# Kernel tuning notes

Measured on AMD Instinct MI355X. Metric: run time of the kernel, lower is better.

Reference implementation:

```python
import jax, jax.numpy as jnp
import numpy as np

N_NODES = 100_000
N_EDGES = 1_000_000
LATENT = 64
HID_ATOM = 256
HID_BOND = 256
RBF_DIM = 32
RBF_DMAX = 10.0
N_ATOM_TYPES = 10
N_CHARGES = 6
N_BOND_ORDERS = 5


def setup_inputs() -> dict:
    key = jax.random.key(0)
    ks = jax.random.split(key, 12)
    positions = jax.random.normal(ks[0], (N_NODES, 3), dtype=jnp.float32) * 5.0
    quantized = jax.random.normal(ks[1], (N_NODES, LATENT), dtype=jnp.float32)
    pair_indices = jax.random.randint(ks[2], (N_EDGES, 2), 0, N_NODES, dtype=jnp.int64)
    s = 0.05
    return {
        "positions": positions,
        "quantized": quantized,
        "pair_indices": pair_indices,
        "aW1": jax.random.normal(ks[3], (LATENT, HID_ATOM), jnp.float32) * s,
        "ab1": jnp.zeros((HID_ATOM,), jnp.float32),
        "aW2": jax.random.normal(ks[4], (HID_ATOM, N_ATOM_TYPES + N_CHARGES), jnp.float32) * s,
        "ab2": jnp.zeros((N_ATOM_TYPES + N_CHARGES,), jnp.float32),
        "bW1": jax.random.normal(ks[5], (LATENT + RBF_DIM, HID_BOND), jnp.float32) * s,
        "bb1": jnp.zeros((HID_BOND,), jnp.float32),
        "bW2": jax.random.normal(ks[6], (HID_BOND, N_BOND_ORDERS), jnp.float32) * s,
        "bb2": jnp.zeros((N_BOND_ORDERS,), jnp.float32),
    }


def _norm_no_nan(x, eps=1e-8):
    # L2 norm over last axis, clamped to avoid NaN gradients at 0
    return jnp.sqrt(jnp.maximum(jnp.sum(x * x, axis=-1), eps))


def _rbf(D, D_min=0.0, D_max=RBF_DMAX, D_count=RBF_DIM):
    mu = jnp.linspace(D_min, D_max, D_count, dtype=D.dtype)  # [D_count]
    sigma = (D_max - D_min) / D_count
    z = (D[..., None] - mu) / sigma
    return jnp.exp(-z * z)  # [E, D_count]


def reference(positions, quantized, pair_indices, aW1, ab1, aW2, ab2, bW1, bb1, bW2, bb2):
    src = pair_indices[:, 0]
    dst = pair_indices[:, 1]
    # pairwise distances -> RBF expansion
    x_i = positions[src]            # [E, 3]
    x_j = positions[dst]
    dists = _rbf(_norm_no_nan(x_i - x_j))  # [E, rbf_dim]
    # atom decoder (per node)
    h = jax.nn.relu(quantized @ aW1 + ab1)
    scalar_logits = h @ aW2 + ab2
    atom_type_logits = scalar_logits[:, :N_ATOM_TYPES]
    atom_charge_logits = scalar_logits[:, N_ATOM_TYPES:]
    # bond decoder (per edge): gathered latent sum concat RBF
    pair_feats = quantized[src] + quantized[dst]           # [E, latent]
    combined = jnp.concatenate([pair_feats, dists], axis=1)  # [E, latent+rbf]
    hb = jax.nn.relu(combined @ bW1 + bb1)
    bond_order_logits = hb @ bW2 + bb2
    return (atom_type_logits, atom_charge_logits, bond_order_logits)
```

## Files before the change

kernel.cpp:

```cpp
#include <hip/hip_runtime.h>
#include <hip/hip_bf16.h>

typedef __bf16 bf16x8 __attribute__((ext_vector_type(8)));
typedef __bf16 bf16x4 __attribute__((ext_vector_type(4)));
typedef float  f32x4  __attribute__((ext_vector_type(4)));

#define N_NODES 100000
#define N_EDGES 1000000
#define LATENT  64
#define HID     256
#define RBF_DIM 32
#define NTYPES  10
#define NCHG    6
#define NBOND   5

#define ATOM_TILES (N_NODES / 32)
#define ANBLK 512

#define ETILE  64
#define ETILES (N_EDGES / ETILE)
#define ENBLK  512

struct __align__(16) ASmem {
    __bf16 qs[32][72];
    __bf16 hsE[32][264];
    float  red[4][2][4][64];
};

template<bool EMIT_QB>
__global__ __launch_bounds__(256, 2) void atom_kernel(
    const float* __restrict__ q,   const float* __restrict__ aW1,
    const float* __restrict__ ab1, const float* __restrict__ aW2,
    const float* __restrict__ ab2, float* __restrict__ outA,
    float* __restrict__ outB,      __bf16* __restrict__ qb)
{
    __shared__ ASmem sm;
    const int t    = threadIdx.x;
    const int w    = t >> 6;
    const int lane = t & 63;
    const int l15  = lane & 15;
    const int hi   = lane >> 4;
    const int wcol = w * 64;

    bf16x8 aw1f[2][4];
    #pragma unroll
    for (int kb = 0; kb < 2; ++kb)
        #pragma unroll
        for (int nt = 0; nt < 4; ++nt) {
            const int nn = wcol + nt * 16 + l15;
            const int k0 = kb * 32 + hi * 8;
            bf16x8 v;
            #pragma unroll
            for (int j = 0; j < 8; ++j) v[j] = (__bf16)aW1[(k0 + j) * HID + nn];
            aw1f[kb][nt] = v;
        }
    bf16x8 aw2f[2];
    #pragma unroll
    for (int kk = 0; kk < 2; ++kk) {
        const int k0 = (w * 2 + kk) * 32 + hi * 8;
        bf16x8 v;
        #pragma unroll
        for (int j = 0; j < 8; ++j) v[j] = (__bf16)aW2[(k0 + j) * 16 + l15];
        aw2f[kk] = v;
    }
    float4 b1v[4];
    #pragma unroll
    for (int nt = 0; nt < 4; ++nt)
        b1v[nt] = *(const float4*)(&ab1[wcol + nt * 16 + hi * 4]);

    const int m_st = t >> 3;
    const int p_st = t & 7;

    for (int tile = blockIdx.x; tile < ATOM_TILES; tile += ANBLK) {
        const int node0 = tile * 32;
        {
            const float* qr = q + (size_t)(node0 + m_st) * 64 + p_st * 8;
            const float4 a0 = *(const float4*)(qr);
            const float4 a1 = *(const float4*)(qr + 4);
            bf16x8 v;
            v[0] = (__bf16)a0.x; v[1] = (__bf16)a0.y; v[2] = (__bf16)a0.z; v[3] = (__bf16)a0.w;
            v[4] = (__bf16)a1.x; v[5] = (__bf16)a1.y; v[6] = (__bf16)a1.z; v[7] = (__bf16)a1.w;
            *(bf16x8*)(&sm.qs[m_st][p_st * 8]) = v;
            if constexpr (EMIT_QB)
                *(bf16x8*)(qb + (size_t)(node0 + m_st) * 64 + p_st * 8) = v;
        }
        __syncthreads();

        f32x4 acc[2][4];
        #pragma unroll
        for (int mt = 0; mt < 2; ++mt)
            #pragma unroll
            for (int nt = 0; nt < 4; ++nt)
                #pragma unroll
                for (int r = 0; r < 4; ++r)
                    acc[mt][nt][r] = ((const float*)&b1v[nt])[r];

        __builtin_amdgcn_s_setprio(1);
        #pragma unroll
        for (int kb = 0; kb < 2; ++kb)
            #pragma unroll
            for (int mt = 0; mt < 2; ++mt) {
                const bf16x8 bq = *(const bf16x8*)((const char*)&sm.qs[0][0]
                                   + (mt * 16 + l15) * 144 + kb * 64 + hi * 16);
                #pragma unroll
                for (int nt = 0; nt < 4; ++nt)
                    acc[mt][nt] = __builtin_amdgcn_mfma_f32_16x16x32_bf16(
                        aw1f[kb][nt], bq, acc[mt][nt], 0, 0, 0);
            }
        __builtin_amdgcn_s_setprio(0);

        #pragma unroll
        for (int mt = 0; mt < 2; ++mt)
            #pragma unroll
            for (int nt = 0; nt < 4; ++nt) {
                bf16x4 hv;
                #pragma unroll
                for (int r = 0; r < 4; ++r)
                    hv[r] = (__bf16)fmaxf(acc[mt][nt][r], 0.f);
                *(bf16x4*)(&sm.hsE[mt * 16 + l15][wcol + nt * 16 + hi * 4]) = hv;
            }
        __syncthreads();

        f32x4 acc2[2];
        {
            f32x4 z = {0.f, 0.f, 0.f, 0.f};
            acc2[0] = z; acc2[1] = z;
        }
        __builtin_amdgcn_s_setprio(1);
        #pragma unroll
        for (int mt = 0; mt < 2; ++mt)
            #pragma unroll
            for (int kk = 0; kk < 2; ++kk) {
                const int kb = w * 2 + kk;
                const bf16x8 af = *(const bf16x8*)((const char*)&sm.hsE[0][0]
                                   + (mt * 16 + l15) * 528 + kb * 64 + hi * 16);
                acc2[mt] = __builtin_amdgcn_mfma_f32_16x16x32_bf16(
                    af, aw2f[kk], acc2[mt], 0, 0, 0);
            }
        __builtin_amdgcn_s_setprio(0);
        #pragma unroll
        for (int mt = 0; mt < 2; ++mt)
            #pragma unroll
            for (int r = 0; r < 4; ++r)
                sm.red[w][mt][r][lane] = acc2[mt][r];
        __syncthreads();

        {
            const int o  = t & 15;
            const int m0 = t >> 4;
            #pragma unroll
            for (int half = 0; half < 2; ++half) {
                const int m  = m0 + half * 16;
                const int mt = m >> 4, rr = m & 15;
                const int hh = rr >> 2, r = rr & 3;
                float s = ab2[o];
                #pragma unroll
                for (int ww = 0; ww < 4; ++ww) s += sm.red[ww][mt][r][hh * 16 + o];
                const int node = node0 + m;
                if (o < NTYPES) outA[node * NTYPES + o] = s;
                else            outB[node * NCHG + (o - NTYPES)] = s;
            }
        }
        __syncthreads();
    }
}

struct __align__(16) ESmem {
    __bf16 comb[ETILE][104];
    __bf16 hsE[ETILE][264];
    __bf16 w2t[16][264];
};

__device__ __forceinline__ void bar_lgkm() {
    asm volatile("s_waitcnt lgkmcnt(0)" ::: "memory");
    __builtin_amdgcn_s_barrier();
}

template<bool USEBF>
__global__ __launch_bounds__(512, 4) void edge_kernel(
    const float* __restrict__ pos, const float* __restrict__ qf,
    const __bf16* __restrict__ qb, const int* __restrict__ pair,
    const float* __restrict__ bW1, const float* __restrict__ bb1,
    const float* __restrict__ bW2, const float* __restrict__ bb2,
    float* __restrict__ outC)
{
    __shared__ ESmem sm;
    const int t    = threadIdx.x;
    const int w    = t >> 6;
    const int lane = t & 63;
    const int l15  = lane & 15;
    const int hi   = lane >> 4;
    const int wcol = w * 32;

    {
        const int o  = t >> 5;
        const int k0 = (t & 31) * 8;
        bf16x8 v;
        #pragma unroll
        for (int j = 0; j < 8; ++j)
            v[j] = (o < NBOND) ? (__bf16)bW2[(k0 + j) * NBOND + o] : (__bf16)0.f;
        *(bf16x8*)(&sm.w2t[o][k0]) = v;
    }

    bf16x8 bw1f[3][2];
    #pragma unroll
    for (int kb = 0; kb < 3; ++kb)
        #pragma unroll
        for (int nt = 0; nt < 2; ++nt) {
            const int nn = wcol + nt * 16 + l15;
            const int k0 = kb * 32 + hi * 8;
            bf16x8 v;
            #pragma unroll
            for (int j = 0; j < 8; ++j) v[j] = (__bf16)bW1[(k0 + j) * HID + nn];
            bw1f[kb][nt] = v;
        }
    float4 b1v[2];
    b1v[0] = *(const float4*)(&bb1[wcol + hi * 4]);
    b1v[1] = *(const float4*)(&bb1[wcol + 16 + hi * 4]);
    const float bb2v = (l15 < NBOND) ? bb2[l15] : 0.f;

    const int e_loc = t >> 3;
    const int p     = t & 7;

    int tile = blockIdx.x;
    int2 pA = ((const int2*)pair)[(size_t)tile * ETILE + e_loc];
    bf16x8 gs, gd;
    float4 fs0, fs1, fd0, fd1;
    float  ps0, ps1, ps2, pd0, pd1, pd2;
    if constexpr (USEBF) {
        gs = *(const bf16x8*)(qb + ((unsigned)pA.x * 64u + (unsigned)(p * 8)));
        gd = *(const bf16x8*)(qb + ((unsigned)pA.y * 64u + (unsigned)(p * 8)));
    } else {
        fs0 = *(const float4*)(qf + ((unsigned)pA.x * 64u + (unsigned)(p * 8)));
        fs1 = *(const float4*)(qf + ((unsigned)pA.x * 64u + (unsigned)(p * 8) + 4u));
        fd0 = *(const float4*)(qf + ((unsigned)pA.y * 64u + (unsigned)(p * 8)));
        fd1 = *(const float4*)(qf + ((unsigned)pA.y * 64u + (unsigned)(p * 8) + 4u));
    }
    ps0 = pos[(unsigned)pA.x * 3u];  ps1 = pos[(unsigned)pA.x * 3u + 1u];  ps2 = pos[(unsigned)pA.x * 3u + 2u];
    pd0 = pos[(unsigned)pA.y * 3u];  pd1 = pos[(unsigned)pA.y * 3u + 1u];  pd2 = pos[(unsigned)pA.y * 3u + 2u];
    {
        const int tn = tile + ENBLK;
        pA = ((const int2*)pair)[(tn < ETILES ? (size_t)tn * ETILE : 0) + e_loc];
    }
    __syncthreads();

    for (; tile < ETILES; tile += ENBLK) {
        const int e0 = tile * ETILE;

        {
            bf16x8 cv;
            if constexpr (USEBF) {
                #pragma unroll
                for (int j = 0; j < 8; ++j)
                    cv[j] = (__bf16)((float)gs[j] + (float)gd[j]);
            } else {
                cv[0] = (__bf16)(fs0.x + fd0.x); cv[1] = (__bf16)(fs0.y + fd0.y);
                cv[2] = (__bf16)(fs0.z + fd0.z); cv[3] = (__bf16)(fs0.w + fd0.w);
                cv[4] = (__bf16)(fs1.x + fd1.x); cv[5] = (__bf16)(fs1.y + fd1.y);
                cv[6] = (__bf16)(fs1.z + fd1.z); cv[7] = (__bf16)(fs1.w + fd1.w);
            }
            *(bf16x8*)(&sm.comb[e_loc][p * 8]) = cv;

            const float dx = ps0 - pd0, dy = ps1 - pd1, dz = ps2 - pd2;
            const float D  = sqrtf(fmaxf(dx * dx + dy * dy + dz * dz, 1e-8f));
            bf16x4 rv;
            #pragma unroll
            for (int j = 0; j < 4; ++j) {
                const float mu = (float)(p * 4 + j) * (10.0f / 31.0f);
                const float z  = (D - mu) * 3.2f;
                rv[j] = (__bf16)__expf(-z * z);
            }
            *(bf16x4*)(&sm.comb[e_loc][64 + p * 4]) = rv;
        }

        {
            const int2 pN = pA;
            if constexpr (USEBF) {
                gs = *(const bf16x8*)(qb + ((unsigned)pN.x * 64u + (unsigned)(p * 8)));
                gd = *(const bf16x8*)(qb + ((unsigned)pN.y * 64u + (unsigned)(p * 8)));
            } else {
                fs0 = *(const float4*)(qf + ((unsigned)pN.x * 64u + (unsigned)(p * 8)));
                fs1 = *(const float4*)(qf + ((unsigned)pN.x * 64u + (unsigned)(p * 8) + 4u));
                fd0 = *(const float4*)(qf + ((unsigned)pN.y * 64u + (unsigned)(p * 8)));
                fd1 = *(const float4*)(qf + ((unsigned)pN.y * 64u + (unsigned)(p * 8) + 4u));
            }
            ps0 = pos[(unsigned)pN.x * 3u];  ps1 = pos[(unsigned)pN.x * 3u + 1u];  ps2 = pos[(unsigned)pN.x * 3u + 2u];
            pd0 = pos[(unsigned)pN.y * 3u];  pd1 = pos[(unsigned)pN.y * 3u + 1u];  pd2 = pos[(unsigned)pN.y * 3u + 2u];
            const int tnn = tile + 2 * ENBLK;
            pA = ((const int2*)pair)[(tnn < ETILES ? (size_t)tnn * ETILE : 0) + e_loc];
        }
        bar_lgkm();

        f32x4 acc[4][2];
        #pragma unroll
        for (int mt = 0; mt < 4; ++mt)
            #pragma unroll
            for (int nt = 0; nt < 2; ++nt)
                #pragma unroll
                for (int r = 0; r < 4; ++r)
                    acc[mt][nt][r] = ((const float*)&b1v[nt])[r];

        __builtin_amdgcn_s_setprio(1);
        #pragma unroll
        for (int kb = 0; kb < 3; ++kb)
            #pragma unroll
            for (int mt = 0; mt < 4; ++mt) {
                const bf16x8 bf = *(const bf16x8*)((const char*)&sm.comb[0][0]
                                   + (mt * 16 + l15) * 208 + kb * 64 + hi * 16);
                acc[mt][0] = __builtin_amdgcn_mfma_f32_16x16x32_bf16(
                    bw1f[kb][0], bf, acc[mt][0], 0, 0, 0);
                acc[mt][1] = __builtin_amdgcn_mfma_f32_16x16x32_bf16(
                    bw1f[kb][1], bf, acc[mt][1], 0, 0, 0);
            }
        __builtin_amdgcn_s_setprio(0);

        #pragma unroll
        for (int mt = 0; mt < 4; ++mt)
            #pragma unroll
            for (int nt = 0; nt < 2; ++nt) {
                bf16x4 hv;
                #pragma unroll
                for (int r = 0; r < 4; ++r)
                    hv[r] = (__bf16)fmaxf(acc[mt][nt][r], 0.f);
                *(bf16x4*)((char*)&sm.hsE[0][0]
                           + (mt * 16 + l15) * 528 + (wcol + nt * 16 + hi * 4) * 2) = hv;
            }
        bar_lgkm();

        if (w < 4) {
            f32x4 a2a, a2b;
            #pragma unroll
            for (int r = 0; r < 4; ++r) { a2a[r] = bb2v; a2b[r] = 0.f; }
            __builtin_amdgcn_s_setprio(1);
            #pragma unroll
            for (int kk = 0; kk < 8; kk += 2) {
                const bf16x8 af0 = *(const bf16x8*)((const char*)&sm.hsE[0][0]
                                    + (w * 16 + l15) * 528 + kk * 64 + hi * 16);
                const bf16x8 bf0 = *(const bf16x8*)((const char*)&sm.w2t[0][0]
                                    + l15 * 528 + kk * 64 + hi * 16);
                a2a = __builtin_amdgcn_mfma_f32_16x16x32_bf16(af0, bf0, a2a, 0, 0, 0);
                const bf16x8 af1 = *(const bf16x8*)((const char*)&sm.hsE[0][0]
                                    + (w * 16 + l15) * 528 + (kk + 1) * 64 + hi * 16);
                const bf16x8 bf1 = *(const bf16x8*)((const char*)&sm.w2t[0][0]
                                    + l15 * 528 + (kk + 1) * 64 + hi * 16);
                a2b = __builtin_amdgcn_mfma_f32_16x16x32_bf16(af1, bf1, a2b, 0, 0, 0);
            }
            __builtin_amdgcn_s_setprio(0);
            if (l15 < NBOND) {
                #pragma unroll
                for (int r = 0; r < 4; ++r)
                    outC[(size_t)(e0 + w * 16 + hi * 4 + r) * NBOND + l15]
                        = a2a[r] + a2b[r];
            }
        }
    }
}

extern "C" void kernel_launch(void* const* d_in, const int* in_sizes, int n_in,
                              void* d_out, int out_size, void* d_ws, size_t ws_size,
                              hipStream_t stream)
{
    const float* pos = (const float*)d_in[0];
    const float* q   = (const float*)d_in[1];
    const int*   pair= (const int*)  d_in[2];
    const float* aW1 = (const float*)d_in[3];
    const float* ab1 = (const float*)d_in[4];
    const float* aW2 = (const float*)d_in[5];
    const float* ab2 = (const float*)d_in[6];
    const float* bW1 = (const float*)d_in[7];
    const float* bb1 = (const float*)d_in[8];
    const float* bW2 = (const float*)d_in[9];
    const float* bb2 = (const float*)d_in[10];

    float* out  = (float*)d_out;
    float* outA = out;
    float* outB = out + (size_t)N_NODES * NTYPES;
    float* outC = out + (size_t)N_NODES * (NTYPES + NCHG);

    const size_t qb_bytes = (size_t)N_NODES * LATENT * sizeof(__bf16);
    const bool use_bf = (ws_size >= qb_bytes);
    __bf16* qb = (__bf16*)d_ws;

    if (use_bf)
        hipLaunchKernelGGL(atom_kernel<true>, dim3(ANBLK), dim3(256), 0, stream,
                           q, aW1, ab1, aW2, ab2, outA, outB, qb);
    else
        hipLaunchKernelGGL(atom_kernel<false>, dim3(ANBLK), dim3(256), 0, stream,
                           q, aW1, ab1, aW2, ab2, outA, outB, qb);

    if (use_bf)
        hipLaunchKernelGGL(edge_kernel<true>, dim3(ENBLK), dim3(512), 0, stream,
                           pos, q, qb, pair, bW1, bb1, bW2, bb2, outC);
    else
        hipLaunchKernelGGL(edge_kernel<false>, dim3(ENBLK), dim3(512), 0, stream,
                           pos, q, qb, pair, bW1, bb1, bW2, bb2, outC);
}
```

Before: 98.99 us.

## Restructure edge kernel into double-buffered 32-edge tiles with per-wave output reduction

```diff
diff --git a/kernel.cpp b/kernel.cpp
--- a/kernel.cpp
+++ b/kernel.cpp
@@ -17,9 +17,9 @@
 #define ATOM_TILES (N_NODES / 32)
 #define ANBLK 512
 
-#define ETILE  64
+#define ETILE  32
 #define ETILES (N_EDGES / ETILE)
-#define ENBLK  512
+#define ENBLK  768
 
 struct __align__(16) ASmem {
     __bf16 qs[32][72];
@@ -95,7 +95,6 @@
                 for (int r = 0; r < 4; ++r)
                     acc[mt][nt][r] = ((const float*)&b1v[nt])[r];
 
-        __builtin_amdgcn_s_setprio(1);
         #pragma unroll
         for (int kb = 0; kb < 2; ++kb)
             #pragma unroll
@@ -107,7 +106,6 @@
                     acc[mt][nt] = __builtin_amdgcn_mfma_f32_16x16x32_bf16(
                         aw1f[kb][nt], bq, acc[mt][nt], 0, 0, 0);
             }
-        __builtin_amdgcn_s_setprio(0);
 
         #pragma unroll
         for (int mt = 0; mt < 2; ++mt)
@@ -126,7 +124,6 @@
             f32x4 z = {0.f, 0.f, 0.f, 0.f};
             acc2[0] = z; acc2[1] = z;
         }
-        __builtin_amdgcn_s_setprio(1);
         #pragma unroll
         for (int mt = 0; mt < 2; ++mt)
             #pragma unroll
@@ -137,7 +134,6 @@
                 acc2[mt] = __builtin_amdgcn_mfma_f32_16x16x32_bf16(
                     af, aw2f[kk], acc2[mt], 0, 0, 0);
             }
-        __builtin_amdgcn_s_setprio(0);
         #pragma unroll
         for (int mt = 0; mt < 2; ++mt)
             #pragma unroll
@@ -166,9 +162,9 @@
 }
 
 struct __align__(16) ESmem {
-    __bf16 comb[ETILE][104];
+    __bf16 comb[2][ETILE][104];
     __bf16 hsE[ETILE][264];
-    __bf16 w2t[16][264];
+    float  red[2][4][2][4][64];
 };
 
 __device__ __forceinline__ void bar_lgkm() {
@@ -177,7 +173,7 @@
 }
 
 template<bool USEBF>
-__global__ __launch_bounds__(512, 4) void edge_kernel(
+__global__ __launch_bounds__(256, 3) void edge_kernel(
     const float* __restrict__ pos, const float* __restrict__ qf,
     const __bf16* __restrict__ qb, const int* __restrict__ pair,
     const float* __restrict__ bW1, const float* __restrict__ bb1,
@@ -190,170 +186,194 @@
     const int lane = t & 63;
     const int l15  = lane & 15;
     const int hi   = lane >> 4;
-    const int wcol = w * 32;
-
-    {
-        const int o  = t >> 5;
-        const int k0 = (t & 31) * 8;
-        bf16x8 v;
-        #pragma unroll
-        for (int j = 0; j < 8; ++j)
-            v[j] = (o < NBOND) ? (__bf16)bW2[(k0 + j) * NBOND + o] : (__bf16)0.f;
-        *(bf16x8*)(&sm.w2t[o][k0]) = v;
-    }
-
-    bf16x8 bw1f[3][2];
+    const int hid0 = w * 64;
+
+    bf16x8 bw1f[3][4];
     #pragma unroll
     for (int kb = 0; kb < 3; ++kb)
         #pragma unroll
-        for (int nt = 0; nt < 2; ++nt) {
-            const int nn = wcol + nt * 16 + l15;
+        for (int nt = 0; nt < 4; ++nt) {
+            const int nn = hid0 + nt * 16 + l15;
             const int k0 = kb * 32 + hi * 8;
             bf16x8 v;
             #pragma unroll
             for (int j = 0; j < 8; ++j) v[j] = (__bf16)bW1[(k0 + j) * HID + nn];
             bw1f[kb][nt] = v;
         }
-    float4 b1v[2];
-    b1v[0] = *(const float4*)(&bb1[wcol + hi * 4]);
-    b1v[1] = *(const float4*)(&bb1[wcol + 16 + hi * 4]);
-    const float bb2v = (l15 < NBOND) ? bb2[l15] : 0.f;
+    bf16x8 w2f[2];
+    #pragma unroll
+    for (int kk = 0; kk < 2; ++kk) {
+        const int k0 = hid0 + kk * 32 + hi * 8;
+        bf16x8 v;
+        #pragma unroll
+        for (int j = 0; j < 8; ++j)
+            v[j] = (l15 < NBOND) ? (__bf16)bW2[(k0 + j) * NBOND + l15] : (__bf16)0.f;
+        w2f[kk] = v;
+    }
+    float4 b1v[4];
+    #pragma unroll
+    for (int nt = 0; nt < 4; ++nt)
+        b1v[nt] = *(const float4*)(&bb1[hid0 + nt * 16 + hi * 4]);
 
     const int e_loc = t >> 3;
     const int p     = t & 7;
 
     int tile = blockIdx.x;
-    int2 pA = ((const int2*)pair)[(size_t)tile * ETILE + e_loc];
     bf16x8 gs, gd;
     float4 fs0, fs1, fd0, fd1;
     float  ps0, ps1, ps2, pd0, pd1, pd2;
-    if constexpr (USEBF) {
-        gs = *(const bf16x8*)(qb + ((unsigned)pA.x * 64u + (unsigned)(p * 8)));
-        gd = *(const bf16x8*)(qb + ((unsigned)pA.y * 64u + (unsigned)(p * 8)));
-    } else {
-        fs0 = *(const float4*)(qf + ((unsigned)pA.x * 64u + (unsigned)(p * 8)));
-        fs1 = *(const float4*)(qf + ((unsigned)pA.x * 64u + (unsigned)(p * 8) + 4u));
-        fd0 = *(const float4*)(qf + ((unsigned)pA.y * 64u + (unsigned)(p * 8)));
-        fd1 = *(const float4*)(qf + ((unsigned)pA.y * 64u + (unsigned)(p * 8) + 4u));
-    }
-    ps0 = pos[(unsigned)pA.x * 3u];  ps1 = pos[(unsigned)pA.x * 3u + 1u];  ps2 = pos[(unsigned)pA.x * 3u + 2u];
-    pd0 = pos[(unsigned)pA.y * 3u];  pd1 = pos[(unsigned)pA.y * 3u + 1u];  pd2 = pos[(unsigned)pA.y * 3u + 2u];
+    int2 pA = ((const int2*)pair)[(size_t)tile * ETILE + e_loc];
+    #define GATHER(pN)                                                            \
+        if constexpr (USEBF) {                                                    \
+            gs = *(const bf16x8*)(qb + ((unsigned)(pN).x * 64u + (unsigned)(p*8)));\
+            gd = *(const bf16x8*)(qb + ((unsigned)(pN).y * 64u + (unsigned)(p*8)));\
+        } else {                                                                  \
+            fs0 = *(const float4*)(qf + ((unsigned)(pN).x * 64u + (unsigned)(p*8)));     \
+            fs1 = *(const float4*)(qf + ((unsigned)(pN).x * 64u + (unsigned)(p*8) + 4u));\
+            fd0 = *(const float4*)(qf + ((unsigned)(pN).y * 64u + (unsigned)(p*8)));     \
+            fd1 = *(const float4*)(qf + ((unsigned)(pN).y * 64u + (unsigned)(p*8) + 4u));\
+        }                                                                         \
+        ps0 = pos[(unsigned)(pN).x * 3u];  ps1 = pos[(unsigned)(pN).x * 3u + 1u]; \
+        ps2 = pos[(unsigned)(pN).x * 3u + 2u];                                    \
+        pd0 = pos[(unsigned)(pN).y * 3u];  pd1 = pos[(unsigned)(pN).y * 3u + 1u]; \
+        pd2 = pos[(unsigned)(pN).y * 3u + 2u];
+
+    #define STAGE(buf)                                                            \
+        {                                                                         \
+            bf16x8 cv;                                                            \
+            if constexpr (USEBF) {                                                \
+                _Pragma("unroll")                                                 \
+                for (int j = 0; j < 8; ++j)                                       \
+                    cv[j] = (__bf16)((float)gs[j] + (float)gd[j]);                \
+            } else {                                                              \
+                cv[0] = (__bf16)(fs0.x + fd0.x); cv[1] = (__bf16)(fs0.y + fd0.y); \
+                cv[2] = (__bf16)(fs0.z + fd0.z); cv[3] = (__bf16)(fs0.w + fd0.w); \
+                cv[4] = (__bf16)(fs1.x + fd1.x); cv[5] = (__bf16)(fs1.y + fd1.y); \
+                cv[6] = (__bf16)(fs1.z + fd1.z); cv[7] = (__bf16)(fs1.w + fd1.w); \
+            }                                                                     \
+            *(bf16x8*)(&sm.comb[buf][e_loc][p * 8]) = cv;                         \
+            const float dx = ps0 - pd0, dy = ps1 - pd1, dz = ps2 - pd2;           \
+            const float D  = sqrtf(fmaxf(dx * dx + dy * dy + dz * dz, 1e-8f));    \
+            bf16x4 rv;                                                            \
+            _Pragma("unroll")                                                     \
+            for (int j = 0; j < 4; ++j) {                                         \
+                const float mu = (float)(p * 4 + j) * (10.0f / 31.0f);            \
+                const float z  = (D - mu) * 3.2f;                                 \
+                rv[j] = (__bf16)__expf(-z * z);                                   \
+            }                                                                     \
+            *(bf16x4*)(&sm.comb[buf][e_loc][64 + p * 4]) = rv;                    \
+        }
+
+    GATHER(pA);
     {
         const int tn = tile + ENBLK;
         pA = ((const int2*)pair)[(tn < ETILES ? (size_t)tn * ETILE : 0) + e_loc];
     }
-    __syncthreads();
+    STAGE(0);
+    GATHER(pA);
+    {
+        const int tn = tile + 2 * ENBLK;
+        pA = ((const int2*)pair)[(tn < ETILES ? (size_t)tn * ETILE : 0) + e_loc];
+    }
+    bar_lgkm();
+
+    int cur = 0;
+    int e0_prev = -1;
 
     for (; tile < ETILES; tile += ENBLK) {
         const int e0 = tile * ETILE;
 
+        if (e0_prev >= 0 && t < 160) {
+            const int m = t / 5, o = t % 5;
+            const int mt = m >> 4, rr = m & 15;
+            const int hh = rr >> 2, r = rr & 3;
+            float s = bb2[o];
+            #pragma unroll
+            for (int ww = 0; ww < 4; ++ww)
+                s += sm.red[cur ^ 1][ww][mt][r][hh * 16 + o];
+            outC[(size_t)(e0_prev + m) * NBOND + o] = s;
+        }
+
+        STAGE(cur ^ 1);
+
+        GATHER(pA);
         {
-            bf16x8 cv;
-            if constexpr (USEBF) {
-                #pragma unroll
-                for (int j = 0; j < 8; ++j)
-                    cv[j] = (__bf16)((float)gs[j] + (float)gd[j]);
-            } else {
-                cv[0] = (__bf16)(fs0.x + fd0.x); cv[1] = (__bf16)(fs0.y + fd0.y);
-                cv[2] = (__bf16)(fs0.z + fd0.z); cv[3] = (__bf16)(fs0.w + fd0.w);
-                cv[4] = (__bf16)(fs1.x + fd1.x); cv[5] = (__bf16)(fs1.y + fd1.y);
-                cv[6] = (__bf16)(fs1.z + fd1.z); cv[7] = (__bf16)(fs1.w + fd1.w);
-            }
-            *(bf16x8*)(&sm.comb[e_loc][p * 8]) = cv;
-
-            const float dx = ps0 - pd0, dy = ps1 - pd1, dz = ps2 - pd2;
-            const float D  = sqrtf(fmaxf(dx * dx + dy * dy + dz * dz, 1e-8f));
-            bf16x4 rv;
-            #pragma unroll
-            for (int j = 0; j < 4; ++j) {
-                const float mu = (float)(p * 4 + j) * (10.0f / 31.0f);
-                const float z  = (D - mu) * 3.2f;
-                rv[j] = (__bf16)__expf(-z * z);
-            }
-            *(bf16x4*)(&sm.comb[e_loc][64 + p * 4]) = rv;
-        }
-
-        {
-            const int2 pN = pA;
-            if constexpr (USEBF) {
-                gs = *(const bf16x8*)(qb + ((unsigned)pN.x * 64u + (unsigned)(p * 8)));
-                gd = *(const bf16x8*)(qb + ((unsigned)pN.y * 64u + (unsigned)(p * 8)));
-            } else {
-                fs0 = *(const float4*)(qf + ((unsigned)pN.x * 64u + (unsigned)(p * 8)));
-                fs1 = *(const float4*)(qf + ((unsigned)pN.x * 64u + (unsigned)(p * 8) + 4u));
-                fd0 = *(const float4*)(qf + ((unsigned)pN.y * 64u + (unsigned)(p * 8)));
-                fd1 = *(const float4*)(qf + ((unsigned)pN.y * 64u + (unsigned)(p * 8) + 4u));
-            }
-            ps0 = pos[(unsigned)pN.x * 3u];  ps1 = pos[(unsigned)pN.x * 3u + 1u];  ps2 = pos[(unsigned)pN.x * 3u + 2u];
-            pd0 = pos[(unsigned)pN.y * 3u];  pd1 = pos[(unsigned)pN.y * 3u + 1u];  pd2 = pos[(unsigned)pN.y * 3u + 2u];
-            const int tnn = tile + 2 * ENBLK;
-            pA = ((const int2*)pair)[(tnn < ETILES ? (size_t)tnn * ETILE : 0) + e_loc];
-        }
-        bar_lgkm();
-
-        f32x4 acc[4][2];
-        #pragma unroll
-        for (int mt = 0; mt < 4; ++mt)
-            #pragma unroll
-            for (int nt = 0; nt < 2; ++nt)
+            const int tn = tile + 3 * ENBLK;
+            pA = ((const int2*)pair)[(tn < ETILES ? (size_t)tn * ETILE : 0) + e_loc];
+        }
+
+        f32x4 acc[2][4];
+        #pragma unroll
+        for (int mt = 0; mt < 2; ++mt)
+            #pragma unroll
+            for (int nt = 0; nt < 4; ++nt)
                 #pragma unroll
                 for (int r = 0; r < 4; ++r)
                     acc[mt][nt][r] = ((const float*)&b1v[nt])[r];
 
-        __builtin_amdgcn_s_setprio(1);
         #pragma unroll
         for (int kb = 0; kb < 3; ++kb)
             #pragma unroll
-            for (int mt = 0; mt < 4; ++mt) {
-                const bf16x8 bf = *(const bf16x8*)((const char*)&sm.comb[0][0]
+            for (int mt = 0; mt < 2; ++mt) {
+                const bf16x8 bf = *(const bf16x8*)((const char*)&sm.comb[cur][0][0]
                                    + (mt * 16 + l15) * 208 + kb * 64 + hi * 16);
-                acc[mt][0] = __builtin_amdgcn_mfma_f32_16x16x32_bf16(
-                    bw1f[kb][0], bf, acc[mt][0], 0, 0, 0);
-                acc[mt][1] = __builtin_amdgcn_mfma_f32_16x16x32_bf16(
-                    bw1f[kb][1], bf, acc[mt][1], 0, 0, 0);
-            }
-        __builtin_amdgcn_s_setprio(0);
-
-        #pragma unroll
-        for (int mt = 0; mt < 4; ++mt)
-            #pragma unroll
-            for (int nt = 0; nt < 2; ++nt) {
+                #pragma unroll
+                for (int nt = 0; nt < 4; ++nt)
+                    acc[mt][nt] = __builtin_amdgcn_mfma_f32_16x16x32_bf16(
+                        bw1f[kb][nt], bf, acc[mt][nt], 0, 0, 0);
+            }
+        #pragma unroll
+        for (int mt = 0; mt < 2; ++mt)
+            #pragma unroll
+            for (int nt = 0; nt < 4; ++nt) {
                 bf16x4 hv;
                 #pragma unroll
                 for (int r = 0; r < 4; ++r)
                     hv[r] = (__bf16)fmaxf(acc[mt][nt][r], 0.f);
                 *(bf16x4*)((char*)&sm.hsE[0][0]
-                           + (mt * 16 + l15) * 528 + (wcol + nt * 16 + hi * 4) * 2) = hv;
-            }
+                           + (mt * 16 + l15) * 528 + (hid0 + nt * 16 + hi * 4) * 2) = hv;
+            }
+
+        {
+            f32x4 acc2[2];
+            {
+                f32x4 z = {0.f, 0.f, 0.f, 0.f};
+                acc2[0] = z; acc2[1] = z;
+            }
+            #pragma unroll
+            for (int mt = 0; mt < 2; ++mt)
+                #pragma unroll
+                for (int kk = 0; kk < 2; ++kk) {
+                    const bf16x8 af = *(const bf16x8*)((const char*)&sm.hsE[0][0]
+                                       + (mt * 16 + l15) * 528
+                                       + (hid0 + kk * 32 + hi * 8) * 2);
+                    acc2[mt] = __builtin_amdgcn_mfma_f32_16x16x32_bf16(
+                        af, w2f[kk], acc2[mt], 0, 0, 0);
+                }
+            #pragma unroll
+            for (int mt = 0; mt < 2; ++mt)
+                #pragma unroll
+                for (int r = 0; r < 4; ++r)
+                    sm.red[cur][w][mt][r][lane] = acc2[mt][r];
+        }
+
+        e0_prev = e0;
         bar_lgkm();
-
-        if (w < 4) {
-            f32x4 a2a, a2b;
-            #pragma unroll
-            for (int r = 0; r < 4; ++r) { a2a[r] = bb2v; a2b[r] = 0.f; }
-            __builtin_amdgcn_s_setprio(1);
-            #pragma unroll
-            for (int kk = 0; kk < 8; kk += 2) {
-                const bf16x8 af0 = *(const bf16x8*)((const char*)&sm.hsE[0][0]
-                                    + (w * 16 + l15) * 528 + kk * 64 + hi * 16);
-                const bf16x8 bf0 = *(const bf16x8*)((const char*)&sm.w2t[0][0]
-                                    + l15 * 528 + kk * 64 + hi * 16);
-                a2a = __builtin_amdgcn_mfma_f32_16x16x32_bf16(af0, bf0, a2a, 0, 0, 0);
-                const bf16x8 af1 = *(const bf16x8*)((const char*)&sm.hsE[0][0]
-                                    + (w * 16 + l15) * 528 + (kk + 1) * 64 + hi * 16);
-                const bf16x8 bf1 = *(const bf16x8*)((const char*)&sm.w2t[0][0]
-                                    + l15 * 528 + (kk + 1) * 64 + hi * 16);
-                a2b = __builtin_amdgcn_mfma_f32_16x16x32_bf16(af1, bf1, a2b, 0, 0, 0);
-            }
-            __builtin_amdgcn_s_setprio(0);
-            if (l15 < NBOND) {
-                #pragma unroll
-                for (int r = 0; r < 4; ++r)
-                    outC[(size_t)(e0 + w * 16 + hi * 4 + r) * NBOND + l15]
-                        = a2a[r] + a2b[r];
-            }
-        }
-    }
+        cur ^= 1;
+    }
+
+    if (e0_prev >= 0 && t < 160) {
+        const int m = t / 5, o = t % 5;
+        const int mt = m >> 4, rr = m & 15;
+        const int hh = rr >> 2, r = rr & 3;
+        float s = bb2[o];
+        #pragma unroll
+        for (int ww = 0; ww < 4; ++ww)
+            s += sm.red[cur ^ 1][ww][mt][r][hh * 16 + o];
+        outC[(size_t)(e0_prev + m) * NBOND + o] = s;
+    }
+    #undef GATHER
+    #undef STAGE
 }
 
 extern "C" void kernel_launch(void* const* d_in, const int* in_sizes, int n_in,
@@ -389,9 +409,9 @@
                            q, aW1, ab1, aW2, ab2, outA, outB, qb);
 
     if (use_bf)
-        hipLaunchKernelGGL(edge_kernel<true>, dim3(ENBLK), dim3(512), 0, stream,
+        hipLaunchKernelGGL(edge_kernel<true>, dim3(ENBLK), dim3(256), 0, stream,
                            pos, q, qb, pair, bW1, bb1, bW2, bb2, outC);
     else
-        hipLaunchKernelGGL(edge_kernel<false>, dim3(ENBLK), dim3(512), 0, stream,
+        hipLaunchKernelGGL(edge_kernel<false>, dim3(ENBLK), dim3(256), 0, stream,
                            pos, q, qb, pair, bW1, bb1, bW2, bb2, outC);
 }
```

Measured after the change: 98.88 us. Within noise of the previous version (-0.1%).
